# Performance work log

Hardware: AMD Instinct MI355X
Metric: run time of the kernel (lower is better)

Reference implementation:

```python
import jax, jax.numpy as jnp
import numpy as np


def setup_inputs() -> dict:
    key = jax.random.key(0)
    k1, k2 = jax.random.split(key)
    B, N, M, D = 32, 1024, 1024, 256
    h1 = jax.random.normal(k1, (B, N, D), dtype=jnp.float32)
    h2 = jax.random.normal(k2, (B, M, D), dtype=jnp.float32)
    return {"h1": h1, "h2": h2}


def reference(h1, h2):
    # Soft Hausdorff over B graph pairs.
    # torch cdist with p=2 here is sum_d |x-y|^2 == squared L2 distance;
    N = h1.shape[1]
    M = h2.shape[1]
    sq1 = jnp.sum(h1 * h1, axis=-1)  # [B, N]
    sq2 = jnp.sum(h2 * h2, axis=-1)  # [B, M]
    cross = jnp.einsum('bnd,bmd->bnm', h1, h2)  # [B, N, M]
    dist = sq1[:, :, None] + sq2[:, None, :] - 2.0 * cross
    dist = jnp.maximum(dist, 0.0)  # guard tiny negative fp noise
    a = jnp.min(dist, axis=1).sum(axis=-1)  # min over N for each col, then sum over M
    b = jnp.min(dist, axis=2).sum(axis=-1)  # min over M for each row, then sum over N
    return (a + b) / min(N, M)  # [B]
```

## Files before the change

### kernel.cpp

```cpp
#include <hip/hip_runtime.h>
#include <hip/hip_bf16.h>
#include <stdint.h>

#define BB 32
#define NN 1024
#define MM 1024
#define DD 256

typedef __attribute__((ext_vector_type(8))) short short8;
typedef __attribute__((ext_vector_type(4))) float floatx4;

__device__ inline unsigned short f2bf(float x) {
    union { __hip_bfloat16 h; unsigned short u; } cv;
    cv.h = __float2bfloat16(x);
    return cv.u;
}
__device__ inline short8 pack8(float4 a, float4 b) {
    short8 o;
    o[0] = f2bf(a.x); o[1] = f2bf(a.y); o[2] = f2bf(a.z); o[3] = f2bf(a.w);
    o[4] = f2bf(b.x); o[5] = f2bf(b.y); o[6] = f2bf(b.z); o[7] = f2bf(b.w);
    return o;
}
__device__ inline void async_copy16(void* lds, const void* g) {
    __builtin_amdgcn_global_load_lds(
        (const __attribute__((address_space(1))) unsigned int*)g,
        (__attribute__((address_space(3))) unsigned int*)lds, 16, 0, 0);
}
__device__ inline void async_copy4(void* lds, const void* g) {
    __builtin_amdgcn_global_load_lds(
        (const __attribute__((address_space(1))) unsigned int*)g,
        (__attribute__((address_space(3))) unsigned int*)lds, 4, 0, 0);
}

__global__ __launch_bounds__(256) void convert_kernel(
        const float* __restrict__ h2, unsigned short* __restrict__ h2b,
        float* __restrict__ sq2, unsigned int* __restrict__ minb) {
    int g = blockIdx.x * 256 + threadIdx.x;
    if (g < 2 * BB * NN) minb[g] = 0x7F800000u;

    int wid  = blockIdx.x * 4 + (threadIdx.x >> 6);
    int lane = threadIdx.x & 63;
    int l5   = lane & 31;
    int row  = wid * 2 + (lane >> 5);

    const float4* p = (const float4*)(h2 + (size_t)row * DD) + l5 * 2;
    float4 a = p[0], c = p[1];

    float s = a.x*a.x + a.y*a.y + a.z*a.z + a.w*a.w
            + c.x*c.x + c.y*c.y + c.z*c.z + c.w*c.w;
    #pragma unroll
    for (int off = 16; off; off >>= 1) s += __shfl_xor(s, off, 64);

    *(short8*)((char*)(h2b + (size_t)row * DD) + l5 * 16) = pack8(a, c);
    if (l5 == 0) sq2[row] = s;
}

__global__ __launch_bounds__(512, 2) void gemm_kernel(
        const float* __restrict__ h1, const unsigned short* __restrict__ h2b,
        const float* __restrict__ sq2,
        unsigned int* __restrict__ rowmin, unsigned int* __restrict__ colmin) {
    __shared__ __align__(16) char pool[98304];
    #define PANEL (pool)
    #define STG   (pool + 32768)
    #define BUF0  (pool + 65536)
    #define BUF1  (pool + 81920)
    #define BUF2  (pool + 0)
    #define BUF3  (pool + 16384)
    __shared__ __align__(16) float  sq1_s[128];
    __shared__ __align__(16) float  sq2_s[1024];
    __shared__ unsigned int cl_s[1024];

    const int b    = blockIdx.x;
    const int tile = blockIdx.y;
    const int n0   = tile * 128;

    const int tid  = threadIdx.x;
    const int wave = tid >> 6;
    const int lane = tid & 63;
    const int wn   = (wave >> 2) * 64;
    const int wm   = (wave & 3) * 32;

    const char* Ag = (const char*)(h1 + ((size_t)b * NN + n0) * DD);
    const char* Bg = (const char*)(h2b + (size_t)b * MM * DD);

    const int krow = lane >> 4;
    const int rrow = lane & 15;
    const int rx   = rrow & 7;
    const int lrow = krow * 4;
    const int lcol = rrow;

    cl_s[tid] = 0x7F800000u; cl_s[tid + 512] = 0x7F800000u;

    #pragma unroll
    for (int t = 0; t < 2; ++t)
        async_copy4((char*)sq2_s + t * 2048 + wave * 256,
                    (const char*)(sq2 + b * MM) + t * 2048 + wave * 256 + lane * 4);

    #define STGQ (pool + 65536)
    #define STAGE_A(q_)                                                       \
        { _Pragma("unroll")                                                   \
          for (int t = 0; t < 4; ++t) {                                       \
            int rl_ = t * 8 + wave;                                           \
            async_copy16(STGQ + rl_ * 1024,                                   \
                Ag + (size_t)((q_) * 32 + rl_) * 1024                         \
                   + ((lane ^ (rl_ & 7)) << 4)); } }

    #pragma unroll 1
    for (int q = 0; q < 4; ++q) {
        STAGE_A(q);
        asm volatile("s_waitcnt vmcnt(0)" ::: "memory");
        __builtin_amdgcn_s_barrier();
        __builtin_amdgcn_sched_barrier(0);
        {
            int prow = tid >> 4;
            int s_   = tid & 15;
            int rg   = q * 32 + prow;
            const char* rp = STGQ + prow * 1024;
            float sum = 0.f;
            #pragma unroll
            for (int jj = 0; jj < 2; ++jj) {
                int g0 = s_ * 4 + jj * 2;
                float4 f0 = *(const float4*)(rp + ((g0 ^ (prow & 7)) << 4));
                float4 f1 = *(const float4*)(rp + (((g0 + 1) ^ (prow & 7)) << 4));
                sum += f0.x*f0.x + f0.y*f0.y + f0.z*f0.z + f0.w*f0.w
                     + f1.x*f1.x + f1.y*f1.y + f1.z*f1.z + f1.w*f1.w;
                int ub = s_ * 2 + jj;
                *(short8*)(PANEL + (size_t)rg * 512 + ((ub ^ (rg & 7)) << 4))
                    = pack8(f0, f1);
            }
            sum += __shfl_xor(sum, 1, 64);
            sum += __shfl_xor(sum, 2, 64);
            sum += __shfl_xor(sum, 4, 64);
            sum += __shfl_xor(sum, 8, 64);
            if (s_ == 0) sq1_s[rg] = sum;
        }
        asm volatile("s_waitcnt lgkmcnt(0)" ::: "memory");
        __builtin_amdgcn_sched_barrier(0);
        __builtin_amdgcn_s_barrier();
        __builtin_amdgcn_sched_barrier(0);
    }

    short8 af[4][8];
    #pragma unroll
    for (int i = 0; i < 4; ++i) {
        #pragma unroll
        for (int kq = 0; kq < 8; ++kq) {
            int u = (kq * 4 + krow) ^ rx;
            af[i][kq] = *(const short8*)(PANEL
                        + (size_t)(wn + i * 16 + rrow) * 512 + (u << 4));
        }
    }
    asm volatile("s_waitcnt lgkmcnt(0)" ::: "memory");
    __builtin_amdgcn_sched_barrier(0);
    __builtin_amdgcn_s_barrier();
    __builtin_amdgcn_sched_barrier(0);

    const int rl  = lane >> 3;
    const int bcu = (lane & 7) ^ rl;
    #define STAGE(mt_, ks_, BUFP)                                             \
        {                                                                     \
            _Pragma("unroll")                                                 \
            for (int c = 0; c < 2; ++c) {                                     \
                int ch_ = wave * 2 + c;                                       \
                int r_  = ch_ * 8 + rl;                                       \
                async_copy16((char*)(BUFP) + ch_ * 1024,                      \
                             Bg + (size_t)((mt_) * 128 + r_) * 512            \
                                + (size_t)(ks_) * 128 + (bcu << 4));          \
            }                                                                 \
        }

    STAGE(0, 0, BUF0);
    STAGE(0, 1, BUF1);
    STAGE(0, 2, BUF2);

    float rmin[4][4];
    #pragma unroll
    for (int i = 0; i < 4; ++i)
        #pragma unroll
        for (int r = 0; r < 4; ++r) rmin[i][r] = 3.0e38f;

    #pragma unroll 1
    for (int mt = 0; mt < 8; ++mt) {
        floatx4 acc[4][2] = {};

        #pragma unroll
        for (int ks = 0; ks < 4; ++ks) {
            if (mt == 7 && ks == 2)      { asm volatile("s_waitcnt vmcnt(2)" ::: "memory"); }
            else if (mt == 7 && ks == 3) { asm volatile("s_waitcnt vmcnt(0)" ::: "memory"); }
            else                         { asm volatile("s_waitcnt vmcnt(4)" ::: "memory"); }
            __builtin_amdgcn_s_barrier();
            __builtin_amdgcn_sched_barrier(0);

            if (ks == 0)          { STAGE(mt,     3, BUF3); }
            else if (mt < 7) {
                if (ks == 1)      { STAGE(mt + 1, 0, BUF0); }
                else if (ks == 2) { STAGE(mt + 1, 1, BUF1); }
                else              { STAGE(mt + 1, 2, BUF2); }
            }

            const char* Bb = (ks == 0) ? BUF0 : (ks == 1) ? BUF1
                           : (ks == 2) ? BUF2 : BUF3;
            __builtin_amdgcn_s_setprio(1);
            #pragma unroll
            for (int kk = 0; kk < 2; ++kk) {
                const int u = ((kk << 2) | krow) ^ rx;
                short8 bfv[2];
                #pragma unroll
                for (int j = 0; j < 2; ++j)
                    bfv[j] = *(const short8*)(Bb
                             + (size_t)(wm + j * 16 + rrow) * 128 + (u << 4));
                #pragma unroll
                for (int i = 0; i < 4; ++i)
                    #pragma unroll
                    for (int j = 0; j < 2; ++j)
                        acc[i][j] = __builtin_amdgcn_mfma_f32_16x16x32_bf16(
                            af[i][ks * 2 + kk], bfv[j], acc[i][j], 0, 0, 0);
            }
            __builtin_amdgcn_s_setprio(0);
        }

        float s2v0 = sq2_s[mt * 128 + wm + lcol];
        float s2v1 = sq2_s[mt * 128 + wm + 16 + lcol];

        float cmin0 = 3.0e38f, cmin1 = 3.0e38f;
        #pragma unroll
        for (int i = 0; i < 4; ++i) {
            float4 s1q = *(const float4*)(&sq1_s[wn + i * 16 + lrow]);
            #pragma unroll
            for (int r = 0; r < 4; ++r) {
                float s1x = ((const float*)&s1q)[r];
                float d0 = fmaxf(s1x + s2v0 - 2.0f * acc[i][0][r], 0.0f);
                float d1 = fmaxf(s1x + s2v1 - 2.0f * acc[i][1][r], 0.0f);
                rmin[i][r] = fminf(rmin[i][r], fminf(d0, d1));
                cmin0 = fminf(cmin0, d0);
                cmin1 = fminf(cmin1, d1);
            }
        }
        cmin0 = fminf(cmin0, __shfl_xor(cmin0, 16, 64));
        cmin0 = fminf(cmin0, __shfl_xor(cmin0, 32, 64));
        cmin1 = fminf(cmin1, __shfl_xor(cmin1, 16, 64));
        cmin1 = fminf(cmin1, __shfl_xor(cmin1, 32, 64));
        if (lane < 16) {
            atomicMin(&cl_s[mt * 128 + wm + lcol],      __float_as_uint(cmin0));
            atomicMin(&cl_s[mt * 128 + wm + 16 + lcol], __float_as_uint(cmin1));
        }
    }

    unsigned int* rm = rowmin + b * NN + n0;
    #pragma unroll
    for (int i = 0; i < 4; ++i) {
        #pragma unroll
        for (int r = 0; r < 4; ++r) {
            float v = rmin[i][r];
            #pragma unroll
            for (int off = 1; off < 16; off <<= 1)
                v = fminf(v, __shfl_xor(v, off, 64));
            if (lcol == 0)
                atomicMin(&rm[wn + i * 16 + lrow + r], __float_as_uint(v));
        }
    }

    __syncthreads();
    unsigned int* cmg = colmin + b * MM;
    atomicMin(&cmg[tid],       cl_s[tid]);
    atomicMin(&cmg[tid + 512], cl_s[tid + 512]);
    #undef STAGE
    #undef STAGE_A
    #undef PANEL
    #undef STG
    #undef STGQ
    #undef BUF0
    #undef BUF1
    #undef BUF2
    #undef BUF3
}

__global__ __launch_bounds__(256) void finalize_kernel(
        const unsigned int* __restrict__ rowmin,
        const unsigned int* __restrict__ colmin,
        float* __restrict__ out) {
    int b = blockIdx.x;
    int tid = threadIdx.x;
    float s = 0.0f;
    for (int i = tid; i < NN; i += 256) s += __uint_as_float(rowmin[b * NN + i]);
    for (int i = tid; i < MM; i += 256) s += __uint_as_float(colmin[b * MM + i]);
    #pragma unroll
    for (int off = 32; off; off >>= 1) s += __shfl_xor(s, off, 64);
    __shared__ float wsum[4];
    if ((tid & 63) == 0) wsum[tid >> 6] = s;
    __syncthreads();
    if (tid == 0) out[b] = (wsum[0] + wsum[1] + wsum[2] + wsum[3]) * (1.0f / 1024.0f);
}

extern "C" void kernel_launch(void* const* d_in, const int* in_sizes, int n_in,
                              void* d_out, int out_size, void* d_ws, size_t ws_size,
                              hipStream_t stream) {
    const float* h1 = (const float*)d_in[0];
    const float* h2 = (const float*)d_in[1];
    float* out = (float*)d_out;

    char* ws = (char*)d_ws;
    unsigned short* h2b = (unsigned short*)ws;
    float* sq2          = (float*)(ws + (size_t)BB * MM * DD * 2);
    unsigned int* rowmin = (unsigned int*)(sq2 + BB * MM);
    unsigned int* colmin = rowmin + BB * NN;

    hipLaunchKernelGGL(convert_kernel, dim3(4096), dim3(256), 0, stream,
                       h2, h2b, sq2, rowmin);

    hipLaunchKernelGGL(gemm_kernel, dim3(BB, 8), dim3(512), 0, stream,
                       h1, h2b, sq2, rowmin, colmin);

    hipLaunchKernelGGL(finalize_kernel, dim3(BB), dim3(256), 0, stream,
                       rowmin, colmin, out);
}
```

Baseline: 49.02 us.

## Load A panel directly into registers and overlap with first B stages

Replaces the four serialized rounds of async LDS staging of the fp32 A tile (each followed by a wait and two barriers) with direct global loads of all four row groups into registers up front. The first two B-tile async copies are then issued before the A data is converted to bf16, written to the LDS panel and reduced to row norms, so the A prologue overlaps with B prefetch. This removes several barriers and an LDS round trip. The cost is 64 extra VGPRs held live during the prologue, which could hurt occupancy under launch bounds of 512 threads with 2 blocks per CU, and the global loads are less coalesced per lane (64-byte contiguous chunks).

```diff
diff --git a/kernel.cpp b/kernel.cpp
--- a/kernel.cpp
+++ b/kernel.cpp
@@ -61,7 +61,6 @@
         unsigned int* __restrict__ rowmin, unsigned int* __restrict__ colmin) {
     __shared__ __align__(16) char pool[98304];
     #define PANEL (pool)
-    #define STG   (pool + 32768)
     #define BUF0  (pool + 65536)
     #define BUF1  (pool + 81920)
     #define BUF2  (pool + 0)
@@ -96,64 +95,15 @@
         async_copy4((char*)sq2_s + t * 2048 + wave * 256,
                     (const char*)(sq2 + b * MM) + t * 2048 + wave * 256 + lane * 4);
 
-    #define STGQ (pool + 65536)
-    #define STAGE_A(q_)                                                       \
-        { _Pragma("unroll")                                                   \
-          for (int t = 0; t < 4; ++t) {                                       \
-            int rl_ = t * 8 + wave;                                           \
-            async_copy16(STGQ + rl_ * 1024,                                   \
-                Ag + (size_t)((q_) * 32 + rl_) * 1024                         \
-                   + ((lane ^ (rl_ & 7)) << 4)); } }
-
-    #pragma unroll 1
+    const int prow = tid >> 4;
+    const int pcol = tid & 15;
+    float4 fa[4][4];
+    #pragma unroll
     for (int q = 0; q < 4; ++q) {
-        STAGE_A(q);
-        asm volatile("s_waitcnt vmcnt(0)" ::: "memory");
-        __builtin_amdgcn_s_barrier();
-        __builtin_amdgcn_sched_barrier(0);
-        {
-            int prow = tid >> 4;
-            int s_   = tid & 15;
-            int rg   = q * 32 + prow;
-            const char* rp = STGQ + prow * 1024;
-            float sum = 0.f;
-            #pragma unroll
-            for (int jj = 0; jj < 2; ++jj) {
-                int g0 = s_ * 4 + jj * 2;
-                float4 f0 = *(const float4*)(rp + ((g0 ^ (prow & 7)) << 4));
-                float4 f1 = *(const float4*)(rp + (((g0 + 1) ^ (prow & 7)) << 4));
-                sum += f0.x*f0.x + f0.y*f0.y + f0.z*f0.z + f0.w*f0.w
-                     + f1.x*f1.x + f1.y*f1.y + f1.z*f1.z + f1.w*f1.w;
-                int ub = s_ * 2 + jj;
-                *(short8*)(PANEL + (size_t)rg * 512 + ((ub ^ (rg & 7)) << 4))
-                    = pack8(f0, f1);
-            }
-            sum += __shfl_xor(sum, 1, 64);
-            sum += __shfl_xor(sum, 2, 64);
-            sum += __shfl_xor(sum, 4, 64);
-            sum += __shfl_xor(sum, 8, 64);
-            if (s_ == 0) sq1_s[rg] = sum;
-        }
-        asm volatile("s_waitcnt lgkmcnt(0)" ::: "memory");
-        __builtin_amdgcn_sched_barrier(0);
-        __builtin_amdgcn_s_barrier();
-        __builtin_amdgcn_sched_barrier(0);
-    }
-
-    short8 af[4][8];
-    #pragma unroll
-    for (int i = 0; i < 4; ++i) {
-        #pragma unroll
-        for (int kq = 0; kq < 8; ++kq) {
-            int u = (kq * 4 + krow) ^ rx;
-            af[i][kq] = *(const short8*)(PANEL
-                        + (size_t)(wn + i * 16 + rrow) * 512 + (u << 4));
-        }
-    }
-    asm volatile("s_waitcnt lgkmcnt(0)" ::: "memory");
-    __builtin_amdgcn_sched_barrier(0);
-    __builtin_amdgcn_s_barrier();
-    __builtin_amdgcn_sched_barrier(0);
+        const char* rp = Ag + (size_t)(q * 32 + prow) * 1024 + pcol * 64;
+        #pragma unroll
+        for (int t = 0; t < 4; ++t) fa[q][t] = *(const float4*)(rp + t * 16);
+    }
 
     const int rl  = lane >> 3;
     const int bcu = (lane & 7) ^ rl;
@@ -171,6 +121,49 @@
 
     STAGE(0, 0, BUF0);
     STAGE(0, 1, BUF1);
+
+    {
+        float sum = 0.f;
+        #pragma unroll
+        for (int q = 0; q < 4; ++q) {
+            int rg = q * 32 + prow;
+            #pragma unroll
+            for (int jj = 0; jj < 2; ++jj) {
+                float4 f0 = fa[q][jj * 2], f1 = fa[q][jj * 2 + 1];
+                sum += f0.x*f0.x + f0.y*f0.y + f0.z*f0.z + f0.w*f0.w
+                     + f1.x*f1.x + f1.y*f1.y + f1.z*f1.z + f1.w*f1.w;
+                int ub = pcol * 2 + jj;
+                *(short8*)(PANEL + (size_t)rg * 512 + ((ub ^ (rg & 7)) << 4))
+                    = pack8(f0, f1);
+            }
+            float s = sum;
+            s += __shfl_xor(s, 1, 64);
+            s += __shfl_xor(s, 2, 64);
+            s += __shfl_xor(s, 4, 64);
+            s += __shfl_xor(s, 8, 64);
+            if (pcol == 0) sq1_s[rg] = s;
+            sum = 0.f;
+        }
+    }
+    asm volatile("s_waitcnt lgkmcnt(0)" ::: "memory");
+    __builtin_amdgcn_sched_barrier(0);
+    __builtin_amdgcn_s_barrier();
+    __builtin_amdgcn_sched_barrier(0);
+
+    short8 af[4][8];
+    #pragma unroll
+    for (int i = 0; i < 4; ++i) {
+        #pragma unroll
+        for (int kq = 0; kq < 8; ++kq) {
+            int u = (kq * 4 + krow) ^ rx;
+            af[i][kq] = *(const short8*)(PANEL
+                        + (size_t)(wn + i * 16 + rrow) * 512 + (u << 4));
+        }
+    }
+    asm volatile("s_waitcnt lgkmcnt(0)" ::: "memory");
+    __builtin_amdgcn_sched_barrier(0);
+    __builtin_amdgcn_s_barrier();
+    __builtin_amdgcn_sched_barrier(0);
     STAGE(0, 2, BUF2);
 
     float rmin[4][4];
@@ -265,10 +258,7 @@
     atomicMin(&cmg[tid],       cl_s[tid]);
     atomicMin(&cmg[tid + 512], cl_s[tid + 512]);
     #undef STAGE
-    #undef STAGE_A
     #undef PANEL
-    #undef STG
-    #undef STGQ
     #undef BUF0
     #undef BUF1
     #undef BUF2
```

Result: no change. 49.01 us (-0.0%).
